# Kernel tuning notes

Hardware: AMD Instinct MI355X
Metric: run time of the kernel (lower is better)

## Reference

```python
import jax, jax.numpy as jnp
import numpy as np

N = 50000
E = 800000
D = 16            # input_dim == hidden_dim == output_dim (required for consistency)
D2 = D * D
HEADS = 4
NEG_SLOPE = 0.2


def _gat_conv(x, src, dst, W, att_src, att_dst, bias):
    """PyG GATConv with concat=False (mean over heads), add_self_loops already applied.
    x: [N, Cin], W: [Cin, H*C], att_*: [H, C], bias: [C]."""
    H, C = att_src.shape
    xh = (x @ W).reshape(N, H, C)                     # [N, H, C]
    a_src = jnp.einsum('nhc,hc->nh', xh, att_src)      # [N, H]
    a_dst = jnp.einsum('nhc,hc->nh', xh, att_dst)
    alpha = jax.nn.leaky_relu(a_src[src] + a_dst[dst], NEG_SLOPE)   # [E, H]
    amax = jax.ops.segment_max(alpha, dst, num_segments=N)
    amax = jnp.where(jnp.isfinite(amax), amax, 0.0)
    ex = jnp.exp(alpha - jax.lax.stop_gradient(amax)[dst])
    denom = jax.ops.segment_sum(ex, dst, num_segments=N)
    coef = ex / (denom[dst] + 1e-16)                  # per-dst softmax over incoming edges
    acc = jnp.zeros((N, C), x.dtype)
    for h in range(H):  # loop over heads to avoid [E, H, C] intermediate
        acc = acc + jax.ops.segment_sum(coef[:, h:h + 1] * xh[src, h], dst, num_segments=N)
    return acc / H + bias


def setup_inputs() -> dict:
    key = jax.random.key(0)
    ks = jax.random.split(key, 20)
    s = lambda k, shape, fan: jax.random.normal(k, shape, jnp.float32) * (1.0 / np.sqrt(fan))
    inp = {
        'mean': jax.random.normal(ks[0], (N, D), jnp.float32),
        'cov': jax.random.normal(ks[1], (N, D, D), jnp.float32),
        'edge_index': jax.random.randint(ks[2], (2, E), 0, N, jnp.int32),
        # gat_mean params
        'W_mean': s(ks[3], (D, HEADS * D), D),
        'att_src_mean': s(ks[4], (HEADS, D), D),
        'att_dst_mean': s(ks[5], (HEADS, D), D),
        'bias_mean': jnp.zeros((D,), jnp.float32),
        # gat_cov params
        'W_cov': s(ks[6], (D2, HEADS * D2), D2),
        'att_src_cov': s(ks[7], (HEADS, D2), D2),
        'att_dst_cov': s(ks[8], (HEADS, D2), D2),
        'bias_cov': jnp.zeros((D2,), jnp.float32),
        # fc_mean: Linear(D,D) -> Linear(D,D)
        'fm_W1': s(ks[9], (D, D), D), 'fm_b1': jnp.zeros((D,), jnp.float32),
        'fm_W2': s(ks[10], (D, D), D), 'fm_b2': jnp.zeros((D,), jnp.float32),
        # fc_cov: Linear(D2,D2) -> Linear(D2,D2)
        'fcv_W1': s(ks[11], (D2, D2), D2), 'fcv_b1': jnp.zeros((D2,), jnp.float32),
        'fcv_W2': s(ks[12], (D2, D2), D2), 'fcv_b2': jnp.zeros((D2,), jnp.float32),
    }
    return inp


def reference(mean, cov, edge_index, W_mean, att_src_mean, att_dst_mean, bias_mean,
              W_cov, att_src_cov, att_dst_cov, bias_cov,
              fm_W1, fm_b1, fm_W2, fm_b2, fcv_W1, fcv_b1, fcv_W2, fcv_b2):
    loops = jnp.arange(N, dtype=edge_index.dtype)
    src = jnp.concatenate([edge_index[0], loops])
    dst = jnp.concatenate([edge_index[1], loops])

    cov_flat = cov.reshape(N, D2)
    mean_agg = _gat_conv(mean, src, dst, W_mean, att_src_mean, att_dst_mean, bias_mean)
    cov_agg = _gat_conv(cov_flat, src, dst, W_cov, att_src_cov, att_dst_cov, bias_cov)

    mean_out = (mean_agg @ fm_W1 + fm_b1) @ fm_W2 + fm_b2
    cov_out = (cov_agg @ fcv_W1 + fcv_b1) @ fcv_W2 + fcv_b2
    return mean_out, cov_out.reshape(N, D, D)
```

## Files before the change

### kernel.cpp

```cpp
#include <hip/hip_runtime.h>

#define NN 50000
#define EE 800000
#define DD 16
#define DD2 256
#define ETOT (EE + NN)
#define NB 196

typedef __bf16 bf16x8 __attribute__((ext_vector_type(8)));
typedef float f32x4 __attribute__((ext_vector_type(4)));
typedef float f32x2 __attribute__((ext_vector_type(2)));

__device__ inline unsigned short f2bf(float f) {
    unsigned int u = __float_as_uint(f);
    return (unsigned short)((u + 0x7FFFu + ((u >> 16) & 1u)) >> 16);
}

__device__ inline void gl2lds16(const void* g, void* l) {
    __builtin_amdgcn_global_load_lds((const __attribute__((address_space(1))) unsigned int*)g,
                                     (__attribute__((address_space(3))) unsigned int*)l, 16, 0, 0);
}

__global__ void k_count(const int* ei, int* counts) {
    int e = blockIdx.x * 256 + threadIdx.x;
    if (e < EE) atomicAdd(&counts[ei[EE + e]], 1);
}

__global__ void k_scan1(const int* counts, int* partial, int* bsum) {
    __shared__ int sh[256];
    int t = threadIdx.x;
    int n = blockIdx.x * 256 + t;
    int v = (n < NN) ? counts[n] + 1 : 0;
    sh[t] = v;
    __syncthreads();
    for (int d = 1; d < 256; d <<= 1) {
        int x = (t >= d) ? sh[t - d] : 0;
        __syncthreads();
        sh[t] += x;
        __syncthreads();
    }
    if (n < NN) partial[n] = sh[t];
    if (t == 255) bsum[blockIdx.x] = sh[255];
}

__global__ void k_scan2(const int* bsum, int* boff) {
    __shared__ int sh[256];
    int t = threadIdx.x;
    int v = (t < NB) ? bsum[t] : 0;
    sh[t] = v;
    __syncthreads();
    for (int d = 1; d < 256; d <<= 1) {
        int x = (t >= d) ? sh[t - d] : 0;
        __syncthreads();
        sh[t] += x;
        __syncthreads();
    }
    if (t < NB) boff[t] = sh[t] - v;
}

__global__ void k_scan3(const int* counts, const int* partial, const int* boff,
                        int* row_start, int* cursor) {
    int n = blockIdx.x * 256 + threadIdx.x;
    if (n < NN) {
        int rs = partial[n] - (counts[n] + 1) + boff[blockIdx.x];
        row_start[n] = rs;
        cursor[n] = rs;
        if (n == NN - 1) row_start[NN] = partial[n] + boff[blockIdx.x];
    }
}

__global__ void k_scatter(const int* ei, int* cursor, int* srt) {
    int i = blockIdx.x * 256 + threadIdx.x;
    if (i >= ETOT) return;
    int s, d;
    if (i < EE) { s = ei[i]; d = ei[EE + i]; }
    else { s = d = i - EE; }
    int pos = atomicAdd(&cursor[d], 1);
    srt[pos] = s;
}

__global__ void k_pre(const float* fcv_W1, const float* fcv_W2, const float* fcv_b1, const float* fcv_b2,
                      const float* fm_W1, const float* fm_W2, const float* fm_b1, const float* fm_b2,
                      const float* W_cov, const float* as_cov, const float* ad_cov,
                      const float* W_mean, const float* as_mean, const float* ad_mean,
                      const float* bias_cov, const float* bias_mean,
                      unsigned short* WpT, float* bpc, float* vcov, float* vmean,
                      float* Wpm, float* bpm) {
    __shared__ float sh[256];
    int b = blockIdx.x, t = threadIdx.x;
    if (b < 1024) {
        int q = b >> 8, i = b & 255;
        const float* wrow = W_cov + (size_t)i * 1024 + q * 256;
        float t1 = 0.f;
        for (int j = 0; j < 256; ++j) t1 += wrow[j] * fcv_W1[j * 256 + t];
        sh[t] = t1;
        __syncthreads();
        float s = 0.f;
        for (int k = 0; k < 256; ++k) s += sh[k] * fcv_W2[k * 256 + t];
        int C = q * 32 + (i >> 3);
        int cs = C ^ (t & 7);
        WpT[(size_t)t * 1024 + cs * 8 + (i & 7)] = f2bf(0.25f * s);
    } else if (b == 1024) {
        float t1 = fcv_b1[t];
        for (int j = 0; j < 256; ++j) t1 += bias_cov[j] * fcv_W1[j * 256 + t];
        sh[t] = t1;
        __syncthreads();
        float s = fcv_b2[t];
        for (int k = 0; k < 256; ++k) s += sh[k] * fcv_W2[k * 256 + t];
        bpc[t] = s;
    } else if (b < 1033) {
        int ch = b - 1025, h = ch & 3;
        const float* att = (ch < 4) ? as_cov : ad_cov;
        int jl = t & 31, i8 = t >> 5;
        float av[8];
#pragma unroll
        for (int jj = 0; jj < 8; ++jj) av[jj] = att[h * 256 + jj * 32 + jl];
        for (int ii = 0; ii < 32; ++ii) {
            int i = ii * 8 + i8;
            const float* wr = W_cov + (size_t)i * 1024 + h * 256;
            float p = 0.f;
#pragma unroll
            for (int jj = 0; jj < 8; ++jj) p += wr[jj * 32 + jl] * av[jj];
#pragma unroll
            for (int off = 16; off; off >>= 1) p += __shfl_xor(p, off);
            if (jl == 0) vcov[ch * 256 + i] = p;
        }
    } else {
        {
            int j = t >> 4, c = t & 15;
            float s = 0.f;
            for (int k = 0; k < 16; ++k) s += fm_W1[j * 16 + k] * fm_W2[k * 16 + c];
            sh[j * 16 + c] = s;
        }
        if (t < 128) {
            int ch = t >> 4, i = t & 15, h = ch & 3;
            const float* att = (ch < 4) ? as_mean : ad_mean;
            float s = 0.f;
            for (int j = 0; j < 16; ++j) s += W_mean[i * 64 + h * 16 + j] * att[h * 16 + j];
            vmean[ch * 16 + i] = s;
        }
        __syncthreads();
#pragma unroll
        for (int r = 0; r < 4; ++r) {
            int idx = r * 256 + t;
            int k = idx >> 4, c = idx & 15, h = k >> 4, i = k & 15;
            float s = 0.f;
            for (int j = 0; j < 16; ++j) s += W_mean[i * 64 + h * 16 + j] * sh[j * 16 + c];
            Wpm[k * 16 + c] = 0.25f * s;
        }
        if (t < 16) {
            float b2 = fm_b2[t];
            for (int k = 0; k < 16; ++k) b2 += fm_b1[k] * fm_W2[k * 16 + t];
            float s = b2;
            for (int j = 0; j < 16; ++j) s += bias_mean[j] * sh[j * 16 + t];
            bpm[t] = s;
        }
    }
}

__global__ void __launch_bounds__(256) k_dots(const float* cov, const float* mean,
                                              const float* vcov, const float* vmean,
                                              float* asrc, float* adst, unsigned short* covb) {
    __shared__ float vc[8 * 256];
    __shared__ float vm[8 * 16];
    int t = threadIdx.x;
    for (int i = t; i < 2048; i += 256) vc[i] = vcov[i];
    if (t < 128) vm[t] = vmean[t];
    __syncthreads();
    int w = t >> 6, lane = t & 63;
    int n = blockIdx.x * 4 + w;
    float4 x = *(const float4*)(cov + (size_t)n * 256 + lane * 4);
    unsigned int u0 = (unsigned int)f2bf(x.x) | ((unsigned int)f2bf(x.y) << 16);
    unsigned int u1 = (unsigned int)f2bf(x.z) | ((unsigned int)f2bf(x.w) << 16);
    *(uint2*)((char*)covb + (size_t)n * 512 + lane * 8) = make_uint2(u0, u1);
    float p[8];
#pragma unroll
    for (int c = 0; c < 8; ++c) {
        float4 v = *(const float4*)&vc[c * 256 + lane * 4];
        p[c] = x.x * v.x + x.y * v.y + x.z * v.z + x.w * v.w;
    }
#pragma unroll
    for (int c = 0; c < 8; ++c)
        for (int off = 32; off; off >>= 1) p[c] += __shfl_xor(p[c], off);
    float xm = (lane < 16) ? mean[(size_t)n * 16 + lane] : 0.f;
    float q[8];
#pragma unroll
    for (int c = 0; c < 8; ++c) {
        q[c] = (lane < 16) ? xm * vm[c * 16 + lane] : 0.f;
        for (int off = 8; off; off >>= 1) q[c] += __shfl_xor(q[c], off);
    }
    if (lane == 0) {
        float4* ps = (float4*)(asrc + (size_t)n * 8);
        ps[0] = make_float4(p[0], p[1], p[2], p[3]);
        ps[1] = make_float4(q[0], q[1], q[2], q[3]);
        float4* pd = (float4*)(adst + (size_t)n * 8);
        pd[0] = make_float4(p[4], p[5], p[6], p[7]);
        pd[1] = make_float4(q[4], q[5], q[6], q[7]);
    }
}

__global__ void __launch_bounds__(256) k_coefdsum(const int* row_start, const int* srt,
                                                  const float* asrc, const float* adst,
                                                  float* exarr, float* dsum) {
    int t = threadIdx.x;
    int n = blockIdx.x * 16 + (t >> 4);
    int sl = t & 15;
    int beg = row_start[n], deg = row_start[n + 1] - beg;
    const float4* pd = (const float4*)(adst + (size_t)n * 8);
    float4 d0 = pd[0], d1 = pd[1];
    float dv[8] = {d0.x, d0.y, d0.z, d0.w, d1.x, d1.y, d1.z, d1.w};
    f32x4 s0 = (f32x4){0.f, 0.f, 0.f, 0.f}, s1 = s0;
    for (int i = sl; i < deg; i += 16) {
        int s = srt[beg + i];
        const float4* pa = (const float4*)(asrc + (size_t)s * 8);
        float4 a0 = pa[0], a1 = pa[1];
        float av[8] = {a0.x, a0.y, a0.z, a0.w, a1.x, a1.y, a1.z, a1.w};
        float ex[8];
#pragma unroll
        for (int c = 0; c < 8; ++c) {
            float al = av[c] + dv[c];
            al = (al >= 0.f) ? al : 0.2f * al;
            ex[c] = __expf(al);
        }
        s0 += (f32x4){ex[0], ex[1], ex[2], ex[3]};
        s1 += (f32x4){ex[4], ex[5], ex[6], ex[7]};
        float4* po = (float4*)(exarr + (size_t)(beg + i) * 8);
        po[0] = make_float4(ex[0], ex[1], ex[2], ex[3]);
        po[1] = make_float4(ex[4], ex[5], ex[6], ex[7]);
    }
#pragma unroll
    for (int off = 1; off < 16; off <<= 1) {
#pragma unroll
        for (int e = 0; e < 4; ++e) {
            s0[e] += __shfl_xor(s0[e], off);
            s1[e] += __shfl_xor(s1[e], off);
        }
    }
    if (sl == 0) {
        f32x4* pds = (f32x4*)(dsum + (size_t)n * 8);
        pds[0] = s0;
        pds[1] = s1;
    }
}

__global__ void __launch_bounds__(256) k_agg(const int* row_start, const int* srt, const float* exarr,
                                             const unsigned short* covb, const float* mean,
                                             const float* dsum,
                                             unsigned short* Ycat, float* Ym) {
    int t = threadIdx.x;
    int w = t >> 6, lane = t & 63;
    int n = blockIdx.x * 4 + w;
    int beg = row_start[n], deg = row_start[n + 1] - beg;
    const int* sp = srt + beg;
    const float* exb = exarr + (size_t)beg * 8;
    int ml = lane & 15;

    f32x2 acc[8];
#pragma unroll
    for (int k = 0; k < 8; ++k) acc[k] = (f32x2){0.f, 0.f};
    float accm[4] = {0, 0, 0, 0};

    int G = deg >> 2;
    int ss[4];
    if (G > 0) {
#pragma unroll
        for (int k = 0; k < 4; ++k) ss[k] = sp[k];
    }
    for (int g = 0; g < G; ++g) {
        int j = g << 2;
        float4 e0[4], e1[4];
#pragma unroll
        for (int k = 0; k < 4; ++k) {
            e0[k] = *(const float4*)(exb + (size_t)(j + k) * 8);
            e1[k] = *(const float4*)(exb + (size_t)(j + k) * 8 + 4);
        }
        uint2 cd[4];
        float mv[4];
#pragma unroll
        for (int k = 0; k < 4; ++k) {
            cd[k] = *(const uint2*)((const char*)covb + (size_t)ss[k] * 512 + lane * 8);
            mv[k] = mean[(size_t)ss[k] * 16 + ml];
        }
        int ns[4];
#pragma unroll
        for (int k = 0; k < 4; ++k) ns[k] = ss[k];
        if (g + 1 < G) {
#pragma unroll
            for (int k = 0; k < 4; ++k) ns[k] = sp[j + 4 + k];
        }
#pragma unroll
        for (int k = 0; k < 4; ++k) {
            f32x2 x0 = (f32x2){__uint_as_float(cd[k].x << 16), __uint_as_float(cd[k].x & 0xffff0000u)};
            f32x2 x1 = (f32x2){__uint_as_float(cd[k].y << 16), __uint_as_float(cd[k].y & 0xffff0000u)};
            float ev[4] = {e0[k].x, e0[k].y, e0[k].z, e0[k].w};
#pragma unroll
            for (int h = 0; h < 4; ++h) {
                f32x2 e2 = (f32x2){ev[h], ev[h]};
                acc[h * 2 + 0] = __builtin_elementwise_fma(e2, x0, acc[h * 2 + 0]);
                acc[h * 2 + 1] = __builtin_elementwise_fma(e2, x1, acc[h * 2 + 1]);
            }
            accm[0] += e1[k].x * mv[k]; accm[1] += e1[k].y * mv[k];
            accm[2] += e1[k].z * mv[k]; accm[3] += e1[k].w * mv[k];
        }
#pragma unroll
        for (int k = 0; k < 4; ++k) ss[k] = ns[k];
    }
    for (int j = G << 2; j < deg; ++j) {
        int sv = sp[j];
        float4 e0 = *(const float4*)(exb + (size_t)j * 8);
        float4 e1 = *(const float4*)(exb + (size_t)j * 8 + 4);
        uint2 cd = *(const uint2*)((const char*)covb + (size_t)sv * 512 + lane * 8);
        float mv = mean[(size_t)sv * 16 + ml];
        f32x2 x0 = (f32x2){__uint_as_float(cd.x << 16), __uint_as_float(cd.x & 0xffff0000u)};
        f32x2 x1 = (f32x2){__uint_as_float(cd.y << 16), __uint_as_float(cd.y & 0xffff0000u)};
        float ev[4] = {e0.x, e0.y, e0.z, e0.w};
#pragma unroll
        for (int h = 0; h < 4; ++h) {
            f32x2 e2 = (f32x2){ev[h], ev[h]};
            acc[h * 2 + 0] = __builtin_elementwise_fma(e2, x0, acc[h * 2 + 0]);
            acc[h * 2 + 1] = __builtin_elementwise_fma(e2, x1, acc[h * 2 + 1]);
        }
        accm[0] += e1.x * mv; accm[1] += e1.y * mv;
        accm[2] += e1.z * mv; accm[3] += e1.w * mv;
    }

    const float4* pds = (const float4*)(dsum + (size_t)n * 8);
    float4 d0 = pds[0], d1 = pds[1];
    float invc[4] = {1.f / (d0.x + 1e-16f), 1.f / (d0.y + 1e-16f),
                     1.f / (d0.z + 1e-16f), 1.f / (d0.w + 1e-16f)};
    float invm[4] = {1.f / (d1.x + 1e-16f), 1.f / (d1.y + 1e-16f),
                     1.f / (d1.z + 1e-16f), 1.f / (d1.w + 1e-16f)};
    char* yrow = (char*)Ycat + (size_t)n * 2048;
    int cbase = lane >> 1, hl = lane & 1, sw = n & 7;
#pragma unroll
    for (int h = 0; h < 4; ++h) {
        float iv = invc[h];
        uint2 pk;
        pk.x = (unsigned int)f2bf(acc[h * 2 + 0].x * iv) | ((unsigned int)f2bf(acc[h * 2 + 0].y * iv) << 16);
        pk.y = (unsigned int)f2bf(acc[h * 2 + 1].x * iv) | ((unsigned int)f2bf(acc[h * 2 + 1].y * iv) << 16);
        int cs = (h * 32 + cbase) ^ sw;
        *(uint2*)(yrow + cs * 16 + hl * 8) = pk;
    }
    if (lane < 16) {
#pragma unroll
        for (int h = 0; h < 4; ++h) Ym[(size_t)n * 64 + h * 16 + lane] = accm[h] * invm[h];
    }
}

__global__ void __launch_bounds__(256) k_gemm(const unsigned short* Ycat, const unsigned short* WpT,
                                              const float* bpc, float* out_cov,
                                              const float* Ym, const float* Wpm, const float* bpm,
                                              float* out_mean) {
    __shared__ __align__(16) unsigned short As[128 * 64];
    __shared__ __align__(16) unsigned short Bs[128 * 64];
    int t = threadIdx.x;
    if (blockIdx.x >= 782) {
        float* wm = (float*)As;
        float* bmv = (float*)Bs;
        for (int i = t; i < 1024; i += 256) wm[i] = Wpm[i];
        if (t < 16) bmv[t] = bpm[t];
        __syncthreads();
        int base = (blockIdx.x - 782) * 64;
        int c = t & 15;
#pragma unroll
        for (int p = 0; p < 4; ++p) {
            int node = base + p * 16 + (t >> 4);
            if (node < NN) {
                const float* yr = Ym + (size_t)node * 64;
                float s = bmv[c];
#pragma unroll
                for (int k = 0; k < 64; ++k) s += yr[k] * wm[k * 16 + c];
                out_mean[(size_t)node * 16 + c] = s;
            }
        }
        return;
    }
    int m0 = (blockIdx.x >> 1) * 128, c0 = (blockIdx.x & 1) * 128;
    int w = t >> 6, lane = t & 63;
    int mg = w >> 1, ng = w & 1;
    int q = lane >> 4, lm = lane & 15;
    f32x4 acc[4][4];
#pragma unroll
    for (int mt = 0; mt < 4; ++mt)
#pragma unroll
        for (int nt = 0; nt < 4; ++nt) acc[mt][nt] = (f32x4){0.f, 0.f, 0.f, 0.f};

    for (int kc = 0; kc < 16; ++kc) {
        int k0 = kc * 64;
#pragma unroll
        for (int i2 = 0; i2 < 4; ++i2) {
            int idx = t + i2 * 256;
            int row = idx >> 3, seg = idx & 7;
            int gm = m0 + row;
            if (gm < NN)
                gl2lds16(Ycat + (size_t)gm * 1024 + k0 + seg * 8, As + idx * 8);
        }
#pragma unroll
        for (int i2 = 0; i2 < 4; ++i2) {
            int idx = t + i2 * 256;
            int col = idx >> 3, seg = idx & 7;
            gl2lds16(WpT + (size_t)(c0 + col) * 1024 + k0 + seg * 8, Bs + idx * 8);
        }
        __syncthreads();
#pragma unroll
        for (int ks = 0; ks < 2; ++ks) {
            bf16x8 af[4], bfr[4];
#pragma unroll
            for (int mt = 0; mt < 4; ++mt) {
                int row = mg * 64 + mt * 16 + lm;
                int ch = (ks * 4 + q) ^ (row & 7);
                af[mt] = *(const bf16x8*)(As + row * 64 + ch * 8);
            }
#pragma unroll
            for (int nt = 0; nt < 4; ++nt) {
                int col = ng * 64 + nt * 16 + lm;
                int ch = (ks * 4 + q) ^ (col & 7);
                bfr[nt] = *(const bf16x8*)(Bs + col * 64 + ch * 8);
            }
#pragma unroll
            for (int mt = 0; mt < 4; ++mt)
#pragma unroll
                for (int nt = 0; nt < 4; ++nt)
                    acc[mt][nt] = __builtin_amdgcn_mfma_f32_16x16x32_bf16(af[mt], bfr[nt], acc[mt][nt], 0, 0, 0);
        }
        __syncthreads();
    }
#pragma unroll
    for (int nt = 0; nt < 4; ++nt) {
        int col = c0 + ng * 64 + nt * 16 + lm;
        float bias = bpc[col];
#pragma unroll
        for (int mt = 0; mt < 4; ++mt) {
#pragma unroll
            for (int e = 0; e < 4; ++e) {
                int r = m0 + mg * 64 + mt * 16 + q * 4 + e;
                if (r < NN)
                    __builtin_nontemporal_store(acc[mt][nt][e] + bias, &out_cov[(size_t)r * 256 + col]);
            }
        }
    }
}

extern "C" void kernel_launch(void* const* d_in, const int* in_sizes, int n_in,
                              void* d_out, int out_size, void* d_ws, size_t ws_size,
                              hipStream_t stream) {
    const float* mean = (const float*)d_in[0];
    const float* cov = (const float*)d_in[1];
    const int* ei = (const int*)d_in[2];
    const float* W_mean = (const float*)d_in[3];
    const float* as_mean = (const float*)d_in[4];
    const float* ad_mean = (const float*)d_in[5];
    const float* bias_mean = (const float*)d_in[6];
    const float* W_cov = (const float*)d_in[7];
    const float* as_cov = (const float*)d_in[8];
    const float* ad_cov = (const float*)d_in[9];
    const float* bias_cov = (const float*)d_in[10];
    const float* fm_W1 = (const float*)d_in[11];
    const float* fm_b1 = (const float*)d_in[12];
    const float* fm_W2 = (const float*)d_in[13];
    const float* fm_b2 = (const float*)d_in[14];
    const float* fcv_W1 = (const float*)d_in[15];
    const float* fcv_b1 = (const float*)d_in[16];
    const float* fcv_W2 = (const float*)d_in[17];
    const float* fcv_b2 = (const float*)d_in[18];

    float* out_mean = (float*)d_out;
    float* out_cov = (float*)d_out + (size_t)NN * DD;

    char* w = (char*)d_ws;
    auto alloc = [&](size_t bytes) -> void* {
        void* p = (void*)w;
        w += (bytes + 255) & ~(size_t)255;
        return p;
    };
    unsigned short* Ycat = (unsigned short*)alloc((size_t)NN * 1024 * 2);
    unsigned short* covb = (unsigned short*)alloc((size_t)NN * 256 * 2);
    float* exarr = (float*)alloc((size_t)ETOT * 8 * 4);
    float* Ym = (float*)alloc((size_t)NN * 64 * 4);
    float* dsum = (float*)alloc((size_t)NN * 8 * 4);
    int* counts = (int*)alloc(NN * 4);
    int* partial = (int*)alloc(NN * 4);
    int* bsum = (int*)alloc(256 * 4);
    int* boff = (int*)alloc(256 * 4);
    int* row_start = (int*)alloc((NN + 1) * 4);
    int* cursor = (int*)alloc(NN * 4);
    int* srt = (int*)alloc((size_t)ETOT * 4);
    float* asrc = (float*)alloc((size_t)NN * 8 * 4);
    float* adst = (float*)alloc((size_t)NN * 8 * 4);
    float* vcov = (float*)alloc(8 * 256 * 4);
    float* vmean = (float*)alloc(8 * 16 * 4);
    unsigned short* WpT = (unsigned short*)alloc(256 * 1024 * 2);
    float* bpc = (float*)alloc(256 * 4);
    float* Wpm = (float*)alloc(64 * 16 * 4);
    float* bpm = (float*)alloc(16 * 4);

    hipMemsetAsync(counts, 0, NN * 4, stream);
    k_count<<<(EE + 255) / 256, 256, 0, stream>>>(ei, counts);
    k_scan1<<<NB, 256, 0, stream>>>(counts, partial, bsum);
    k_scan2<<<1, 256, 0, stream>>>(bsum, boff);
    k_scan3<<<NB, 256, 0, stream>>>(counts, partial, boff, row_start, cursor);
    k_scatter<<<(ETOT + 255) / 256, 256, 0, stream>>>(ei, cursor, srt);
    k_pre<<<1034, 256, 0, stream>>>(fcv_W1, fcv_W2, fcv_b1, fcv_b2, fm_W1, fm_W2, fm_b1, fm_b2,
                                    W_cov, as_cov, ad_cov, W_mean, as_mean, ad_mean,
                                    bias_cov, bias_mean, WpT, bpc, vcov, vmean, Wpm, bpm);
    k_dots<<<NN / 4, 256, 0, stream>>>(cov, mean, vcov, vmean, asrc, adst, covb);
    k_coefdsum<<<3125, 256, 0, stream>>>(row_start, srt, asrc, adst, exarr, dsum);
    k_agg<<<NN / 4, 256, 0, stream>>>(row_start, srt, exarr, covb, mean, dsum, Ycat, Ym);
    k_gemm<<<782 + 782, 256, 0, stream>>>(Ycat, WpT, bpc, out_cov, Ym, Wpm, bpm, out_mean);
}
```

Baseline: 472.3 us.

## Fuse attention coefficient computation into aggregation and merge scan kernels

```diff
diff --git a/kernel.cpp b/kernel.cpp
--- a/kernel.cpp
+++ b/kernel.cpp
@@ -43,7 +43,8 @@
     if (t == 255) bsum[blockIdx.x] = sh[255];
 }
 
-__global__ void k_scan2(const int* bsum, int* boff) {
+__global__ void k_scan3(const int* counts, const int* partial, const int* bsum,
+                        int* row_start, int* cursor) {
     __shared__ int sh[256];
     int t = threadIdx.x;
     int v = (t < NB) ? bsum[t] : 0;
@@ -55,17 +56,13 @@
         sh[t] += x;
         __syncthreads();
     }
-    if (t < NB) boff[t] = sh[t] - v;
-}
-
-__global__ void k_scan3(const int* counts, const int* partial, const int* boff,
-                        int* row_start, int* cursor) {
-    int n = blockIdx.x * 256 + threadIdx.x;
+    int boff = (blockIdx.x == 0) ? 0 : sh[blockIdx.x - 1];
+    int n = blockIdx.x * 256 + t;
     if (n < NN) {
-        int rs = partial[n] - (counts[n] + 1) + boff[blockIdx.x];
+        int rs = partial[n] - (counts[n] + 1) + boff;
         row_start[n] = rs;
         cursor[n] = rs;
-        if (n == NN - 1) row_start[NN] = partial[n] + boff[blockIdx.x];
+        if (n == NN - 1) row_start[NN] = partial[n] + boff;
     }
 }
 
@@ -199,137 +196,91 @@
     }
 }
 
-__global__ void __launch_bounds__(256) k_coefdsum(const int* row_start, const int* srt,
-                                                  const float* asrc, const float* adst,
-                                                  float* exarr, float* dsum) {
-    int t = threadIdx.x;
-    int n = blockIdx.x * 16 + (t >> 4);
-    int sl = t & 15;
-    int beg = row_start[n], deg = row_start[n + 1] - beg;
-    const float4* pd = (const float4*)(adst + (size_t)n * 8);
-    float4 d0 = pd[0], d1 = pd[1];
-    float dv[8] = {d0.x, d0.y, d0.z, d0.w, d1.x, d1.y, d1.z, d1.w};
-    f32x4 s0 = (f32x4){0.f, 0.f, 0.f, 0.f}, s1 = s0;
-    for (int i = sl; i < deg; i += 16) {
-        int s = srt[beg + i];
-        const float4* pa = (const float4*)(asrc + (size_t)s * 8);
-        float4 a0 = pa[0], a1 = pa[1];
-        float av[8] = {a0.x, a0.y, a0.z, a0.w, a1.x, a1.y, a1.z, a1.w};
-        float ex[8];
-#pragma unroll
-        for (int c = 0; c < 8; ++c) {
-            float al = av[c] + dv[c];
-            al = (al >= 0.f) ? al : 0.2f * al;
-            ex[c] = __expf(al);
-        }
-        s0 += (f32x4){ex[0], ex[1], ex[2], ex[3]};
-        s1 += (f32x4){ex[4], ex[5], ex[6], ex[7]};
-        float4* po = (float4*)(exarr + (size_t)(beg + i) * 8);
-        po[0] = make_float4(ex[0], ex[1], ex[2], ex[3]);
-        po[1] = make_float4(ex[4], ex[5], ex[6], ex[7]);
-    }
-#pragma unroll
-    for (int off = 1; off < 16; off <<= 1) {
-#pragma unroll
-        for (int e = 0; e < 4; ++e) {
-            s0[e] += __shfl_xor(s0[e], off);
-            s1[e] += __shfl_xor(s1[e], off);
-        }
-    }
-    if (sl == 0) {
-        f32x4* pds = (f32x4*)(dsum + (size_t)n * 8);
-        pds[0] = s0;
-        pds[1] = s1;
-    }
-}
-
-__global__ void __launch_bounds__(256) k_agg(const int* row_start, const int* srt, const float* exarr,
+__global__ void __launch_bounds__(256) k_agg(const int* row_start, const int* srt,
+                                             const float* asrc, const float* adst,
                                              const unsigned short* covb, const float* mean,
-                                             const float* dsum,
                                              unsigned short* Ycat, float* Ym) {
+    __shared__ float exbuf[4][64][8];
     int t = threadIdx.x;
     int w = t >> 6, lane = t & 63;
     int n = blockIdx.x * 4 + w;
     int beg = row_start[n], deg = row_start[n + 1] - beg;
-    const int* sp = srt + beg;
-    const float* exb = exarr + (size_t)beg * 8;
     int ml = lane & 15;
-
+    float ad[8];
+    {
+        const float4* pd = (const float4*)(adst + (size_t)n * 8);
+        float4 d0 = pd[0], d1 = pd[1];
+        ad[0] = d0.x; ad[1] = d0.y; ad[2] = d0.z; ad[3] = d0.w;
+        ad[4] = d1.x; ad[5] = d1.y; ad[6] = d1.z; ad[7] = d1.w;
+    }
     f32x2 acc[8];
 #pragma unroll
     for (int k = 0; k < 8; ++k) acc[k] = (f32x2){0.f, 0.f};
     float accm[4] = {0, 0, 0, 0};
-
-    int G = deg >> 2;
-    int ss[4];
-    if (G > 0) {
-#pragma unroll
-        for (int k = 0; k < 4; ++k) ss[k] = sp[k];
-    }
-    for (int g = 0; g < G; ++g) {
-        int j = g << 2;
-        float4 e0[4], e1[4];
-#pragma unroll
-        for (int k = 0; k < 4; ++k) {
-            e0[k] = *(const float4*)(exb + (size_t)(j + k) * 8);
-            e1[k] = *(const float4*)(exb + (size_t)(j + k) * 8 + 4);
-        }
-        uint2 cd[4];
-        float mv[4];
-#pragma unroll
-        for (int k = 0; k < 4; ++k) {
-            cd[k] = *(const uint2*)((const char*)covb + (size_t)ss[k] * 512 + lane * 8);
-            mv[k] = mean[(size_t)ss[k] * 16 + ml];
-        }
-        int ns[4];
-#pragma unroll
-        for (int k = 0; k < 4; ++k) ns[k] = ss[k];
-        if (g + 1 < G) {
-#pragma unroll
-            for (int k = 0; k < 4; ++k) ns[k] = sp[j + 4 + k];
-        }
-#pragma unroll
-        for (int k = 0; k < 4; ++k) {
-            f32x2 x0 = (f32x2){__uint_as_float(cd[k].x << 16), __uint_as_float(cd[k].x & 0xffff0000u)};
-            f32x2 x1 = (f32x2){__uint_as_float(cd[k].y << 16), __uint_as_float(cd[k].y & 0xffff0000u)};
-            float ev[4] = {e0[k].x, e0[k].y, e0[k].z, e0[k].w};
-#pragma unroll
-            for (int h = 0; h < 4; ++h) {
-                f32x2 e2 = (f32x2){ev[h], ev[h]};
-                acc[h * 2 + 0] = __builtin_elementwise_fma(e2, x0, acc[h * 2 + 0]);
-                acc[h * 2 + 1] = __builtin_elementwise_fma(e2, x1, acc[h * 2 + 1]);
-            }
-            accm[0] += e1[k].x * mv[k]; accm[1] += e1[k].y * mv[k];
-            accm[2] += e1[k].z * mv[k]; accm[3] += e1[k].w * mv[k];
-        }
-#pragma unroll
-        for (int k = 0; k < 4; ++k) ss[k] = ns[k];
-    }
-    for (int j = G << 2; j < deg; ++j) {
-        int sv = sp[j];
-        float4 e0 = *(const float4*)(exb + (size_t)j * 8);
-        float4 e1 = *(const float4*)(exb + (size_t)j * 8 + 4);
-        uint2 cd = *(const uint2*)((const char*)covb + (size_t)sv * 512 + lane * 8);
-        float mv = mean[(size_t)sv * 16 + ml];
-        f32x2 x0 = (f32x2){__uint_as_float(cd.x << 16), __uint_as_float(cd.x & 0xffff0000u)};
-        f32x2 x1 = (f32x2){__uint_as_float(cd.y << 16), __uint_as_float(cd.y & 0xffff0000u)};
-        float ev[4] = {e0.x, e0.y, e0.z, e0.w};
-#pragma unroll
-        for (int h = 0; h < 4; ++h) {
-            f32x2 e2 = (f32x2){ev[h], ev[h]};
-            acc[h * 2 + 0] = __builtin_elementwise_fma(e2, x0, acc[h * 2 + 0]);
-            acc[h * 2 + 1] = __builtin_elementwise_fma(e2, x1, acc[h * 2 + 1]);
-        }
-        accm[0] += e1.x * mv; accm[1] += e1.y * mv;
-        accm[2] += e1.z * mv; accm[3] += e1.w * mv;
-    }
-
-    const float4* pds = (const float4*)(dsum + (size_t)n * 8);
-    float4 d0 = pds[0], d1 = pds[1];
-    float invc[4] = {1.f / (d0.x + 1e-16f), 1.f / (d0.y + 1e-16f),
-                     1.f / (d0.z + 1e-16f), 1.f / (d0.w + 1e-16f)};
-    float invm[4] = {1.f / (d1.x + 1e-16f), 1.f / (d1.y + 1e-16f),
-                     1.f / (d1.z + 1e-16f), 1.f / (d1.w + 1e-16f)};
+    float ds8[8] = {0, 0, 0, 0, 0, 0, 0, 0};
+
+    for (int base = 0; base < deg; base += 64) {
+        int i = base + lane;
+        bool valid = i < deg;
+        int s0 = srt[beg + (valid ? i : (deg - 1))];
+        const float4* pa = (const float4*)(asrc + (size_t)s0 * 8);
+        float4 a0 = pa[0], a1 = pa[1];
+        float av[8] = {a0.x, a0.y, a0.z, a0.w, a1.x, a1.y, a1.z, a1.w};
+        float ex8[8];
+#pragma unroll
+        for (int c = 0; c < 8; ++c) {
+            float al = av[c] + ad[c];
+            al = (al >= 0.f) ? al : 0.2f * al;
+            float e = __expf(al);
+            e = valid ? e : 0.f;
+            ex8[c] = e;
+            ds8[c] += e;
+        }
+        *(float4*)&exbuf[w][lane][0] = make_float4(ex8[0], ex8[1], ex8[2], ex8[3]);
+        *(float4*)&exbuf[w][lane][4] = make_float4(ex8[4], ex8[5], ex8[6], ex8[7]);
+        int cnt = min(64, deg - base);
+        int cnt4 = (cnt + 3) & ~3;
+        for (int jp = 0; jp < cnt4; jp += 4) {
+            int se[4];
+            float4 e0[4], e1[4];
+#pragma unroll
+            for (int k = 0; k < 4; ++k) se[k] = __shfl(s0, jp + k);
+#pragma unroll
+            for (int k = 0; k < 4; ++k) {
+                e0[k] = *(const float4*)&exbuf[w][jp + k][0];
+                e1[k] = *(const float4*)&exbuf[w][jp + k][4];
+            }
+            uint2 cd[4];
+            float mv[4];
+#pragma unroll
+            for (int k = 0; k < 4; ++k) {
+                cd[k] = *(const uint2*)((const char*)covb + (size_t)se[k] * 512 + lane * 8);
+                mv[k] = mean[(size_t)se[k] * 16 + ml];
+            }
+#pragma unroll
+            for (int k = 0; k < 4; ++k) {
+                f32x2 x0 = (f32x2){__uint_as_float(cd[k].x << 16), __uint_as_float(cd[k].x & 0xffff0000u)};
+                f32x2 x1 = (f32x2){__uint_as_float(cd[k].y << 16), __uint_as_float(cd[k].y & 0xffff0000u)};
+                float ev[4] = {e0[k].x, e0[k].y, e0[k].z, e0[k].w};
+#pragma unroll
+                for (int h = 0; h < 4; ++h) {
+                    f32x2 e2 = (f32x2){ev[h], ev[h]};
+                    acc[h * 2 + 0] = __builtin_elementwise_fma(e2, x0, acc[h * 2 + 0]);
+                    acc[h * 2 + 1] = __builtin_elementwise_fma(e2, x1, acc[h * 2 + 1]);
+                }
+                accm[0] += e1[k].x * mv[k]; accm[1] += e1[k].y * mv[k];
+                accm[2] += e1[k].z * mv[k]; accm[3] += e1[k].w * mv[k];
+            }
+        }
+    }
+#pragma unroll
+    for (int c = 0; c < 8; ++c)
+        for (int off = 32; off; off >>= 1) ds8[c] += __shfl_xor(ds8[c], off);
+
+    float invc[4] = {1.f / (ds8[0] + 1e-16f), 1.f / (ds8[1] + 1e-16f),
+                     1.f / (ds8[2] + 1e-16f), 1.f / (ds8[3] + 1e-16f)};
+    float invm[4] = {1.f / (ds8[4] + 1e-16f), 1.f / (ds8[5] + 1e-16f),
+                     1.f / (ds8[6] + 1e-16f), 1.f / (ds8[7] + 1e-16f)};
     char* yrow = (char*)Ycat + (size_t)n * 2048;
     int cbase = lane >> 1, hl = lane & 1, sw = n & 7;
 #pragma unroll
@@ -360,10 +311,10 @@
         for (int i = t; i < 1024; i += 256) wm[i] = Wpm[i];
         if (t < 16) bmv[t] = bpm[t];
         __syncthreads();
-        int base = (blockIdx.x - 782) * 64;
+        int base = (blockIdx.x - 782) * 256;
         int c = t & 15;
 #pragma unroll
-        for (int p = 0; p < 4; ++p) {
+        for (int p = 0; p < 16; ++p) {
             int node = base + p * 16 + (t >> 4);
             if (node < NN) {
                 const float* yr = Ym + (size_t)node * 64;
@@ -475,13 +426,10 @@
     };
     unsigned short* Ycat = (unsigned short*)alloc((size_t)NN * 1024 * 2);
     unsigned short* covb = (unsigned short*)alloc((size_t)NN * 256 * 2);
-    float* exarr = (float*)alloc((size_t)ETOT * 8 * 4);
     float* Ym = (float*)alloc((size_t)NN * 64 * 4);
-    float* dsum = (float*)alloc((size_t)NN * 8 * 4);
     int* counts = (int*)alloc(NN * 4);
     int* partial = (int*)alloc(NN * 4);
     int* bsum = (int*)alloc(256 * 4);
-    int* boff = (int*)alloc(256 * 4);
     int* row_start = (int*)alloc((NN + 1) * 4);
     int* cursor = (int*)alloc(NN * 4);
     int* srt = (int*)alloc((size_t)ETOT * 4);
@@ -497,14 +445,12 @@
     hipMemsetAsync(counts, 0, NN * 4, stream);
     k_count<<<(EE + 255) / 256, 256, 0, stream>>>(ei, counts);
     k_scan1<<<NB, 256, 0, stream>>>(counts, partial, bsum);
-    k_scan2<<<1, 256, 0, stream>>>(bsum, boff);
-    k_scan3<<<NB, 256, 0, stream>>>(counts, partial, boff, row_start, cursor);
+    k_scan3<<<NB, 256, 0, stream>>>(counts, partial, bsum, row_start, cursor);
     k_scatter<<<(ETOT + 255) / 256, 256, 0, stream>>>(ei, cursor, srt);
     k_pre<<<1034, 256, 0, stream>>>(fcv_W1, fcv_W2, fcv_b1, fcv_b2, fm_W1, fm_W2, fm_b1, fm_b2,
                                     W_cov, as_cov, ad_cov, W_mean, as_mean, ad_mean,
                                     bias_cov, bias_mean, WpT, bpc, vcov, vmean, Wpm, bpm);
     k_dots<<<NN / 4, 256, 0, stream>>>(cov, mean, vcov, vmean, asrc, adst, covb);
-    k_coefdsum<<<3125, 256, 0, stream>>>(row_start, srt, asrc, adst, exarr, dsum);
-    k_agg<<<NN / 4, 256, 0, stream>>>(row_start, srt, exarr, covb, mean, dsum, Ycat, Ym);
-    k_gemm<<<782 + 782, 256, 0, stream>>>(Ycat, WpT, bpc, out_cov, Ym, Wpm, bpm, out_mean);
-}
+    k_agg<<<NN / 4, 256, 0, stream>>>(row_start, srt, asrc, adst, covb, mean, Ycat, Ym);
+    k_gemm<<<782 + 196, 256, 0, stream>>>(Ycat, WpT, bpc, out_cov, Ym, Wpm, bpm, out_mean);
+}
```

Result: no change. 464.5 us (-1.7%).
